# Optimization experiments

Measured on AMD Instinct MI355X. Metric: run time of the kernel, lower is better.

Reference implementation:

```python
import jax, jax.numpy as jnp
import numpy as np

# Dims: batch N, time T, joints V=9, K=5 adjacency partitions (spatial strategy, max_hop=2),
# in channels 16, out channels = coords = 3, temporal kernel 9 (ConvTranspose, stride 1, pad 4).
N, T, V, C_IN, C_OUT, K, KT = 256, 2048, 9, 16, 3, 5, 9


def setup_inputs() -> dict:
    key = jax.random.key(0)
    ks = jax.random.split(key, 6)
    pose_feats = jax.random.normal(ks[0], (N, T, V * C_IN), jnp.float32)
    # Fixed (non-trainable) multi-partition normalized adjacency A2: [K, V, V].
    # Graph values come from ted_db constants in the repo; stand-in: row-normalized random.
    A = jax.random.uniform(ks[1], (K, V, V), jnp.float32)
    A = A / jnp.sum(A, axis=-1, keepdims=True)
    # GCN 1x1 conv: in -> K*C_OUT channels
    W_gcn = jax.random.normal(ks[2], (K, C_OUT, C_IN), jnp.float32) * (1.0 / np.sqrt(C_IN))
    b_gcn = jax.random.normal(ks[3], (K, C_OUT), jnp.float32) * 0.02
    # Temporal ConvTranspose2d(C_OUT, C_OUT, kernel=(9,1), stride=(1,1), padding=(4,0));
    # torch weight layout [in, out, kH, kW]
    W_tcn = jax.random.normal(ks[4], (C_OUT, C_OUT, KT, 1), jnp.float32) * (1.0 / np.sqrt(C_OUT * KT))
    b_tcn = jax.random.normal(ks[5], (C_OUT,), jnp.float32) * 0.02
    return {"pose_feats": pose_feats, "A": A, "W_gcn": W_gcn, "b_gcn": b_gcn,
            "W_tcn": W_tcn, "b_tcn": b_tcn}


def _st_gcn_transpose(x, A, W_gcn, b_gcn, W_tcn, b_tcn):
    # x: [n, c_in, t, v]
    # 1x1 conv to K*C_OUT channels, then adjacency contraction over partitions k
    y = jnp.einsum('nctv,koc->nkotv', x, W_gcn) + b_gcn[None, :, :, None, None]
    y = jnp.einsum('nkotv,kvw->notw', y, A)  # [n, c_out, t, v]
    # temporal transposed conv, kernel (9,1), stride 1, torch padding 4 -> jax pad (4,4)
    y = jax.lax.conv_transpose(y, W_tcn, strides=(1, 1), padding=[(4, 4), (0, 0)],
                               dimension_numbers=('NCHW', 'IOHW', 'NCHW'),
                               transpose_kernel=True)
    y = y + b_tcn[None, :, None, None]
    return jax.nn.leaky_relu(y, 0.01)


def reference(pose_feats, A, W_gcn, b_gcn, W_tcn, b_tcn):
    n, t, f = pose_feats.shape
    x = pose_feats.reshape(n, t, V, C_IN).transpose(0, 3, 1, 2)  # [n, c_in, t, v]
    y = _st_gcn_transpose(x, A, W_gcn, b_gcn, W_tcn, b_tcn)      # [n, c_out, t, v]
    return y.transpose(0, 2, 3, 1).reshape(n, t, V * C_OUT)       # [n, t, 27]
```

## Files before the change

kernel.cpp:

```cpp
#include <hip/hip_runtime.h>

typedef short short8 __attribute__((ext_vector_type(8)));
typedef float f32x4  __attribute__((ext_vector_type(4)));

constexpr int N_    = 256;
constexpr int T_    = 2048;
constexpr int V_    = 9;
constexpr int FIN_  = 144;
constexpr int J_    = 27;
constexpr int KT_   = 9;
constexpr int THREADS_ = 256;
constexpr int TILE_  = 248;
constexpr int NTILE_ = 9;
constexpr int XSTRIDE_B = 336;
constexpr int XBUF_B  = 64 * XSTRIDE_B;
constexpr int ZROWS_  = 256;
constexpr int ZS_     = 28;
constexpr int SMEM_B  = XBUF_B + ZROWS_ * ZS_ * 4;

constexpr int BF_OFF_F = 0;
constexpr int B0_OFF   = 2560;
constexpr int WT_OFF   = 2587;
constexpr int BT_OFF   = 2668;

__device__ __forceinline__ unsigned short bf16_rne(float x) {
    unsigned u = __float_as_uint(x);
    u = (u + 0x7FFFu + ((u >> 16) & 1u)) >> 16;
    return (unsigned short)u;
}
__device__ __forceinline__ unsigned pk2(float a, float b) {
    return (unsigned)bf16_rne(a) | ((unsigned)bf16_rne(b) << 16);
}

__global__ void setup_weights(const float* __restrict__ A,
                              const float* __restrict__ Wg,
                              const float* __restrict__ bg,
                              const float* __restrict__ Wt_in,
                              const float* __restrict__ bt,
                              float* __restrict__ ws) {
    __shared__ float Wc[FIN_ * J_];
    const int tid = threadIdx.x;
    for (int idx = tid; idx < FIN_ * J_; idx += 256) {
        const int f = idx / J_, j = idx % J_;
        const int v = f >> 4, c = f & 15;
        const int w = j / 3, o = j % 3;
        float s = 0.f;
        #pragma unroll
        for (int k = 0; k < 5; ++k)
            s += Wg[(k * 3 + o) * 16 + c] * A[(k * 9 + v) * 9 + w];
        Wc[idx] = s;
    }
    __syncthreads();
    unsigned short* bfp = (unsigned short*)(ws + BF_OFF_F);
    for (int i = tid; i < 5120; i += 256) {
        const int e = i & 7, lane = (i >> 3) & 63, nt = (i >> 9) & 1, s = i >> 10;
        const int k = s * 32 + (lane >> 4) * 8 + e;
        const int n = nt * 16 + (lane & 15);
        const float val = (k < FIN_ && n < J_) ? Wc[k * J_ + n] : 0.f;
        bfp[i] = bf16_rne(val);
    }
    if (tid < J_) {
        const int w = tid / 3, o = tid % 3;
        float s = 0.f;
        #pragma unroll
        for (int k = 0; k < 5; ++k) {
            float cs = 0.f;
            #pragma unroll
            for (int v = 0; v < V_; ++v) cs += A[(k * 9 + v) * 9 + w];
            s += bg[k * 3 + o] * cs;
        }
        ws[B0_OFF + tid] = s;
    }
    if (tid < 81) {
        const int o = tid / 27, r = tid % 27, o2 = r / 9, dd = r % 9;
        ws[WT_OFF + tid] = Wt_in[(o2 * 3 + o) * 9 + (8 - dd)];
    }
    if (tid < 3) ws[BT_OFF + tid] = bt[tid];
}

__global__ __launch_bounds__(THREADS_, 3) void fused_stgcn(const float* __restrict__ pose,
                                                           const float* __restrict__ cw,
                                                           float* __restrict__ out) {
    __shared__ __align__(16) unsigned char smem[SMEM_B];
    float* zbuf = (float*)(smem + XBUF_B);

    const int tid  = threadIdx.x;
    const int bid  = blockIdx.x;
    const int nb   = bid / NTILE_;
    const int tile = bid % NTILE_;
    const int t0   = tile * TILE_;
    const int lane = tid & 63;
    const int wv   = tid >> 6;
    const int g8   = lane >> 4;
    const int j0   = lane & 15;
    const size_t nrow0 = (size_t)nb * T_;

    auto WB = []() {
        asm volatile("s_waitcnt lgkmcnt(0)" ::: "memory");
        __builtin_amdgcn_s_barrier();
        asm volatile("" ::: "memory");
    };

    auto issue = [&](int h, float4* ld) {
        #pragma unroll
        for (int q = 0; q < 9; ++q) {
            const int fidx = q * THREADS_ + tid;
            const int r = fidx / 36, c4 = fidx % 36;
            const int text = t0 - 4 + h * 64 + r;
            const bool ok = (text >= 0 && text < T_);
            const float* p = pose + (nrow0 + (size_t)(ok ? text : 0)) * FIN_ + c4 * 4;
            ld[q] = ok ? *(const float4*)p : make_float4(0.f, 0.f, 0.f, 0.f);
        }
    };
    auto stage = [&](const float4* ld) {
        #pragma unroll
        for (int q = 0; q < 9; ++q) {
            const int fidx = q * THREADS_ + tid;
            const int r = fidx / 36, c4 = fidx % 36;
            uint2 u;
            u.x = pk2(ld[q].x, ld[q].y);
            u.y = pk2(ld[q].z, ld[q].w);
            *(uint2*)(smem + r * XSTRIDE_B + c4 * 8) = u;
        }
    };

    float4 lda[9], ldb[9];
    issue(0, lda);

    for (int i = tid; i < 512; i += THREADS_) {
        const int r = i >> 3, w = i & 7;
        *(float*)(smem + r * XSTRIDE_B + 288 + w * 4) = 0.f;
    }
    short8 bfrag[5][2];
    {
        const short8* bsrc = (const short8*)(cw + BF_OFF_F);
        #pragma unroll
        for (int s = 0; s < 5; ++s)
            #pragma unroll
            for (int nt = 0; nt < 2; ++nt)
                bfrag[s][nt] = bsrc[(s * 2 + nt) * 64 + lane];
    }
    const float b0n0 = cw[B0_OFF + j0];
    const float b0n1 = (j0 < 11) ? cw[B0_OFF + 16 + j0] : 0.f;

    #pragma unroll
    for (int h = 0; h < 4; ++h) {
        float4* cur = (h & 1) ? ldb : lda;
        float4* nxt = (h & 1) ? lda : ldb;
        if (h < 3) issue(h + 1, nxt);
        stage(cur);
        WB();

        const unsigned char* abase = smem + (wv * 16 + j0) * XSTRIDE_B;
        f32x4 acc0 = {0.f, 0.f, 0.f, 0.f};
        f32x4 acc1 = {0.f, 0.f, 0.f, 0.f};
        #pragma unroll
        for (int s = 0; s < 5; ++s) {
            const short8 af = *(const short8*)(abase + s * 64 + g8 * 16);
            acc0 = __builtin_amdgcn_mfma_f32_16x16x32_bf16(af, bfrag[s][0], acc0, 0, 0, 0);
            acc1 = __builtin_amdgcn_mfma_f32_16x16x32_bf16(af, bfrag[s][1], acc1, 0, 0, 0);
        }
        #pragma unroll
        for (int r = 0; r < 4; ++r) {
            const int zrow = h * 64 + wv * 16 + g8 * 4 + r;
            const int text = t0 - 4 + zrow;
            const bool okz = (text >= 0 && text < T_);
            zbuf[zrow * ZS_ + j0] = okz ? acc0[r] + b0n0 : 0.f;
            if (j0 < 11)
                zbuf[zrow * ZS_ + 16 + j0] = okz ? acc1[r] + b0n1 : 0.f;
        }
        WB();
    }

    const int rows_out = min(TILE_, T_ - t0);
    float oacc[J_];
    if (tid < rows_out) {
        #pragma unroll
        for (int w = 0; w < V_; ++w)
            #pragma unroll
            for (int o2 = 0; o2 < 3; ++o2)
                oacc[w * 3 + o2] = cw[BT_OFF + o2];
        #pragma unroll
        for (int dd = 0; dd < KT_; ++dd) {
            union { f32x4 v4[7]; float f[28]; } zu;
            const f32x4* zp = (const f32x4*)&zbuf[(tid + dd) * ZS_];
            #pragma unroll
            for (int c = 0; c < 7; ++c) zu.v4[c] = zp[c];
            #pragma unroll
            for (int o = 0; o < 3; ++o) {
                #pragma unroll
                for (int o2 = 0; o2 < 3; ++o2) {
                    const float wt = cw[WT_OFF + o * 27 + o2 * 9 + dd];
                    #pragma unroll
                    for (int w = 0; w < V_; ++w)
                        oacc[w * 3 + o2] = fmaf(zu.f[w * 3 + o], wt, oacc[w * 3 + o2]);
                }
            }
        }
        #pragma unroll
        for (int j = 0; j < J_; ++j) oacc[j] = fmaxf(oacc[j], 0.01f * oacc[j]);
    }
    WB();
    if (tid < rows_out) {
        #pragma unroll
        for (int j = 0; j < J_; ++j) zbuf[tid * J_ + j] = oacc[j];
    }
    WB();

    const int total4 = (rows_out * J_) / 4;
    float4* dst4 = (float4*)(out + (nrow0 + t0) * J_);
    const float4* src4 = (const float4*)zbuf;
    for (int idx = tid; idx < total4; idx += THREADS_)
        dst4[idx] = src4[idx];
}

extern "C" void kernel_launch(void* const* d_in, const int* in_sizes, int n_in,
                              void* d_out, int out_size, void* d_ws, size_t ws_size,
                              hipStream_t stream) {
    const float* pose = (const float*)d_in[0];
    const float* A    = (const float*)d_in[1];
    const float* Wg   = (const float*)d_in[2];
    const float* bg   = (const float*)d_in[3];
    const float* Wt   = (const float*)d_in[4];
    const float* bt   = (const float*)d_in[5];
    float* ws   = (float*)d_ws;
    float* outp = (float*)d_out;

    setup_weights<<<1, 256, 0, stream>>>(A, Wg, bg, Wt, bt, ws);
    fused_stgcn<<<N_ * NTILE_, THREADS_, 0, stream>>>(pose, ws, outp);
}
```

Baseline: 87.69 us.

## Fold weight setup into main kernel, store z in bf16, raise occupancy

Drops the separate single-block setup kernel: every block now computes the combined GCN weight matrix, bias and bf16 MFMA fragments itself from the raw inputs, using shared memory as scratch. The intermediate z buffer is stored as bf16 instead of fp32, halving its shared-memory footprint. The load double-buffer becomes a single buffer and the stage loop is no longer unrolled, which together with the smaller shared memory lets launch bounds ask for 4 blocks per CU. The cost is redundant weight precomputation in all 2304 blocks, less overlap between global loads and staging, and extra bf16 rounding on z.

```diff
diff --git a/kernel.cpp b/kernel.cpp
--- a/kernel.cpp
+++ b/kernel.cpp
@@ -14,14 +14,9 @@
 constexpr int NTILE_ = 9;
 constexpr int XSTRIDE_B = 336;
 constexpr int XBUF_B  = 64 * XSTRIDE_B;
-constexpr int ZROWS_  = 256;
-constexpr int ZS_     = 28;
-constexpr int SMEM_B  = XBUF_B + ZROWS_ * ZS_ * 4;
-
-constexpr int BF_OFF_F = 0;
-constexpr int B0_OFF   = 2560;
-constexpr int WT_OFF   = 2587;
-constexpr int BT_OFF   = 2668;
+constexpr int ZSU_    = 28;
+constexpr int ZBUF_B  = 256 * ZSU_ * 2;
+constexpr int SMEM_B  = XBUF_B + ZBUF_B;
 
 __device__ __forceinline__ unsigned short bf16_rne(float x) {
     unsigned u = __float_as_uint(x);
@@ -31,58 +26,18 @@
 __device__ __forceinline__ unsigned pk2(float a, float b) {
     return (unsigned)bf16_rne(a) | ((unsigned)bf16_rne(b) << 16);
 }
-
-__global__ void setup_weights(const float* __restrict__ A,
-                              const float* __restrict__ Wg,
-                              const float* __restrict__ bg,
-                              const float* __restrict__ Wt_in,
-                              const float* __restrict__ bt,
-                              float* __restrict__ ws) {
-    __shared__ float Wc[FIN_ * J_];
-    const int tid = threadIdx.x;
-    for (int idx = tid; idx < FIN_ * J_; idx += 256) {
-        const int f = idx / J_, j = idx % J_;
-        const int v = f >> 4, c = f & 15;
-        const int w = j / 3, o = j % 3;
-        float s = 0.f;
-        #pragma unroll
-        for (int k = 0; k < 5; ++k)
-            s += Wg[(k * 3 + o) * 16 + c] * A[(k * 9 + v) * 9 + w];
-        Wc[idx] = s;
-    }
-    __syncthreads();
-    unsigned short* bfp = (unsigned short*)(ws + BF_OFF_F);
-    for (int i = tid; i < 5120; i += 256) {
-        const int e = i & 7, lane = (i >> 3) & 63, nt = (i >> 9) & 1, s = i >> 10;
-        const int k = s * 32 + (lane >> 4) * 8 + e;
-        const int n = nt * 16 + (lane & 15);
-        const float val = (k < FIN_ && n < J_) ? Wc[k * J_ + n] : 0.f;
-        bfp[i] = bf16_rne(val);
-    }
-    if (tid < J_) {
-        const int w = tid / 3, o = tid % 3;
-        float s = 0.f;
-        #pragma unroll
-        for (int k = 0; k < 5; ++k) {
-            float cs = 0.f;
-            #pragma unroll
-            for (int v = 0; v < V_; ++v) cs += A[(k * 9 + v) * 9 + w];
-            s += bg[k * 3 + o] * cs;
-        }
-        ws[B0_OFF + tid] = s;
-    }
-    if (tid < 81) {
-        const int o = tid / 27, r = tid % 27, o2 = r / 9, dd = r % 9;
-        ws[WT_OFF + tid] = Wt_in[(o2 * 3 + o) * 9 + (8 - dd)];
-    }
-    if (tid < 3) ws[BT_OFF + tid] = bt[tid];
-}
-
-__global__ __launch_bounds__(THREADS_, 3) void fused_stgcn(const float* __restrict__ pose,
-                                                           const float* __restrict__ cw,
+__device__ __forceinline__ float bflo(unsigned u) { return __uint_as_float(u << 16); }
+__device__ __forceinline__ float bfhi(unsigned u) { return __uint_as_float(u & 0xFFFF0000u); }
+
+__global__ __launch_bounds__(THREADS_, 4) void fused_stgcn(const float* __restrict__ pose,
+                                                           const float* __restrict__ Ain,
+                                                           const float* __restrict__ Wg,
+                                                           const float* __restrict__ bg,
+                                                           const float* __restrict__ Wt_in,
+                                                           const float* __restrict__ bt,
                                                            float* __restrict__ out) {
     __shared__ __align__(16) unsigned char smem[SMEM_B];
-    float* zbuf = (float*)(smem + XBUF_B);
+    unsigned short* zb = (unsigned short*)(smem + XBUF_B);
 
     const int tid  = threadIdx.x;
     const int bid  = blockIdx.x;
@@ -124,31 +79,73 @@
         }
     };
 
-    float4 lda[9], ldb[9];
-    issue(0, lda);
-
+    float4 ld[9];
+    issue(0, ld);
+
+    float* wc = (float*)smem;
+    for (int idx = tid; idx < FIN_ * J_; idx += THREADS_) {
+        const int f = idx / J_, j = idx % J_;
+        const int v = f >> 4, c = f & 15;
+        const int w = j / 3, o = j % 3;
+        float s = 0.f;
+        #pragma unroll
+        for (int k = 0; k < 5; ++k)
+            s += Wg[(k * 3 + o) * 16 + c] * Ain[(k * 9 + v) * 9 + w];
+        wc[idx] = s;
+    }
+    float b0n0, b0n1 = 0.f;
+    {
+        const int n0 = j0, w0 = n0 / 3, o0 = n0 % 3;
+        float s0 = 0.f;
+        #pragma unroll
+        for (int k = 0; k < 5; ++k) {
+            float cs = 0.f;
+            #pragma unroll
+            for (int v = 0; v < V_; ++v) cs += Ain[(k * 9 + v) * 9 + w0];
+            s0 += bg[k * 3 + o0] * cs;
+        }
+        b0n0 = s0;
+        if (j0 < 11) {
+            const int n1 = 16 + j0, w1 = n1 / 3, o1 = n1 % 3;
+            float s1 = 0.f;
+            #pragma unroll
+            for (int k = 0; k < 5; ++k) {
+                float cs = 0.f;
+                #pragma unroll
+                for (int v = 0; v < V_; ++v) cs += Ain[(k * 9 + v) * 9 + w1];
+                s1 += bg[k * 3 + o1] * cs;
+            }
+            b0n1 = s1;
+        }
+    }
+    WB();
+    short8 bfrag[5][2];
+    #pragma unroll
+    for (int s = 0; s < 5; ++s) {
+        #pragma unroll
+        for (int nt = 0; nt < 2; ++nt) {
+            const int n = nt * 16 + j0;
+            union { unsigned u[4]; short8 s8; } cvu;
+            #pragma unroll
+            for (int ep = 0; ep < 4; ++ep) {
+                const int k0 = s * 32 + g8 * 8 + ep * 2;
+                const float v0 = (k0 < FIN_ && n < J_)     ? wc[k0 * J_ + n]       : 0.f;
+                const float v1 = (k0 + 1 < FIN_ && n < J_) ? wc[(k0 + 1) * J_ + n] : 0.f;
+                cvu.u[ep] = pk2(v0, v1);
+            }
+            bfrag[s][nt] = cvu.s8;
+        }
+    }
+    WB();
     for (int i = tid; i < 512; i += THREADS_) {
         const int r = i >> 3, w = i & 7;
         *(float*)(smem + r * XSTRIDE_B + 288 + w * 4) = 0.f;
     }
-    short8 bfrag[5][2];
-    {
-        const short8* bsrc = (const short8*)(cw + BF_OFF_F);
-        #pragma unroll
-        for (int s = 0; s < 5; ++s)
-            #pragma unroll
-            for (int nt = 0; nt < 2; ++nt)
-                bfrag[s][nt] = bsrc[(s * 2 + nt) * 64 + lane];
-    }
-    const float b0n0 = cw[B0_OFF + j0];
-    const float b0n1 = (j0 < 11) ? cw[B0_OFF + 16 + j0] : 0.f;
-
-    #pragma unroll
+
+    #pragma unroll 1
     for (int h = 0; h < 4; ++h) {
-        float4* cur = (h & 1) ? ldb : lda;
-        float4* nxt = (h & 1) ? lda : ldb;
-        if (h < 3) issue(h + 1, nxt);
-        stage(cur);
+        stage(ld);
+        if (h < 3) issue(h + 1, ld);
         WB();
 
         const unsigned char* abase = smem + (wv * 16 + j0) * XSTRIDE_B;
@@ -165,9 +162,9 @@
             const int zrow = h * 64 + wv * 16 + g8 * 4 + r;
             const int text = t0 - 4 + zrow;
             const bool okz = (text >= 0 && text < T_);
-            zbuf[zrow * ZS_ + j0] = okz ? acc0[r] + b0n0 : 0.f;
+            zb[zrow * ZSU_ + j0] = bf16_rne(okz ? acc0[r] + b0n0 : 0.f);
             if (j0 < 11)
-                zbuf[zrow * ZS_ + 16 + j0] = okz ? acc1[r] + b0n1 : 0.f;
+                zb[zrow * ZSU_ + 16 + j0] = bf16_rne(okz ? acc1[r] + b0n1 : 0.f);
         }
         WB();
     }
@@ -179,21 +176,25 @@
         for (int w = 0; w < V_; ++w)
             #pragma unroll
             for (int o2 = 0; o2 < 3; ++o2)
-                oacc[w * 3 + o2] = cw[BT_OFF + o2];
+                oacc[w * 3 + o2] = bt[o2];
         #pragma unroll
         for (int dd = 0; dd < KT_; ++dd) {
-            union { f32x4 v4[7]; float f[28]; } zu;
-            const f32x4* zp = (const f32x4*)&zbuf[(tid + dd) * ZS_];
-            #pragma unroll
-            for (int c = 0; c < 7; ++c) zu.v4[c] = zp[c];
+            const unsigned* zp = (const unsigned*)(zb + (tid + dd) * ZSU_);
+            float zf[28];
+            #pragma unroll
+            for (int c = 0; c < 14; ++c) {
+                const unsigned u = zp[c];
+                zf[2 * c]     = bflo(u);
+                zf[2 * c + 1] = bfhi(u);
+            }
             #pragma unroll
             for (int o = 0; o < 3; ++o) {
                 #pragma unroll
                 for (int o2 = 0; o2 < 3; ++o2) {
-                    const float wt = cw[WT_OFF + o * 27 + o2 * 9 + dd];
+                    const float wt = Wt_in[(o2 * 3 + o) * KT_ + (KT_ - 1 - dd)];
                     #pragma unroll
                     for (int w = 0; w < V_; ++w)
-                        oacc[w * 3 + o2] = fmaf(zu.f[w * 3 + o], wt, oacc[w * 3 + o2]);
+                        oacc[w * 3 + o2] = fmaf(zf[w * 3 + o], wt, oacc[w * 3 + o2]);
                 }
             }
         }
@@ -201,15 +202,16 @@
         for (int j = 0; j < J_; ++j) oacc[j] = fmaxf(oacc[j], 0.01f * oacc[j]);
     }
     WB();
+    float* rp = (float*)smem;
     if (tid < rows_out) {
         #pragma unroll
-        for (int j = 0; j < J_; ++j) zbuf[tid * J_ + j] = oacc[j];
+        for (int j = 0; j < J_; ++j) rp[tid * J_ + j] = oacc[j];
     }
     WB();
 
     const int total4 = (rows_out * J_) / 4;
     float4* dst4 = (float4*)(out + (nrow0 + t0) * J_);
-    const float4* src4 = (const float4*)zbuf;
+    const float4* src4 = (const float4*)rp;
     for (int idx = tid; idx < total4; idx += THREADS_)
         dst4[idx] = src4[idx];
 }
@@ -223,9 +225,7 @@
     const float* bg   = (const float*)d_in[3];
     const float* Wt   = (const float*)d_in[4];
     const float* bt   = (const float*)d_in[5];
-    float* ws   = (float*)d_ws;
     float* outp = (float*)d_out;
 
-    setup_weights<<<1, 256, 0, stream>>>(A, Wg, bg, Wt, bt, ws);
-    fused_stgcn<<<N_ * NTILE_, THREADS_, 0, stream>>>(pose, ws, outp);
-}
+    fused_stgcn<<<N_ * NTILE_, THREADS_, 0, stream>>>(pose, A, Wg, bg, Wt, bt, outp);
+}
```

Measured after the change: 208.2 us. 137% more time.
